# Optimization experiments

Measured on AMD Instinct MI355X. Metric: run time of the kernel, lower is better.

## Reference

```python
import jax, jax.numpy as jnp
import numpy as np

B, L, P, D = 512, 32, 256, 2


def hungarian(cost):
    """Min-cost assignment on an [n,n] numpy cost matrix (rows=pred, cols=target).
    Returns col[row]: target index assigned to each pred row (same as scipy
    linear_sum_assignment col_ind). Jonker-Volgenant style augmenting path."""
    n = cost.shape[0]
    INF = 1e18
    u = np.zeros(n + 1)
    v = np.zeros(n + 1)
    p = np.zeros(n + 1, dtype=np.int64)
    way = np.zeros(n + 1, dtype=np.int64)
    for i in range(1, n + 1):
        p[0] = i
        j0 = 0
        minv = np.full(n + 1, INF)
        used = np.zeros(n + 1, dtype=bool)
        while True:
            used[j0] = True
            i0 = p[j0]
            free = ~used[1:]
            cur = cost[i0 - 1, :] - u[i0] - v[1:]
            upd = free & (cur < minv[1:])
            m1 = minv[1:]
            m1[upd] = cur[upd]
            w1 = way[1:]
            w1[upd] = j0
            mfree = np.where(free, m1, INF)
            j1 = int(np.argmin(mfree)) + 1
            delta = mfree[j1 - 1]
            u[p[used]] += delta
            v[used] -= delta
            m1[free] -= delta
            j0 = j1
            if p[j0] == 0:
                break
        while j0:
            j1 = way[j0]
            p[j0] = p[j1]
            j0 = j1
    col = np.zeros(n, dtype=np.int64)
    for j in range(1, n + 1):
        col[p[j] - 1] = j - 1
    return col


def match_targets_np(pred_flat, tgt_flat, n_lines):
    """pred_flat/tgt_flat: np [B, L, P*D]; n_lines: np int [B].
    Replicates match_lines_sequence: Hungarian on pairwise squared L2 over the
    first n valid lines; unmatched rows stay zero (they are masked in the loss)."""
    out = np.zeros_like(pred_flat)
    for b in range(pred_flat.shape[0]):
        n = int(n_lines[b])
        if n == 1:
            out[b] = tgt_flat[b]
            continue
        pr = pred_flat[b, :n]
        tg = tgt_flat[b, :n]
        cost = ((pr[:, None, :] - tg[None, :, :]) ** 2).sum(-1)  # [pred, target]
        col = hungarian(cost)
        out[b, :n] = tgt_flat[b][col]
    return out


def setup_inputs() -> dict:
    key = jax.random.key(0)
    ks = jax.random.split(key, 5)
    point_pos_pred = jax.random.normal(ks[0], (B, L, P, D), jnp.float32)
    target_pos = jax.random.normal(ks[1], (B, L, P, D), jnp.float32)
    # probabilities in (0,1), bounded away from 0 so -log is finite
    line_prob_pred = jax.random.uniform(ks[2], (B, L, 2), jnp.float32) * 0.9 + 0.05
    n_lines = jax.random.randint(ks[3], (B,), 1, L + 1)
    line_masks = (jnp.arange(L)[None, :] < n_lines[:, None]).astype(jnp.float32)
    clf_line = jax.random.randint(ks[4], (B, L), 0, 2).astype(jnp.int32)
    point_masks = (line_masks[:, :, None] * jnp.ones((1, 1, P), jnp.float32))
    return {
        "point_pos_pred": point_pos_pred,
        "line_prob_pred": line_prob_pred,
        "target_pos": target_pos,
        "line_masks": line_masks,
        "clf_line": clf_line,
        "point_masks": point_masks,
    }


def reference(point_pos_pred, line_prob_pred, target_pos, line_masks, clf_line, point_masks):
    # --- Hungarian matching (host-side, non-differentiable, as in the original) ---
    pp = np.asarray(point_pos_pred).reshape(B, L, P * D)
    tp = np.asarray(target_pos).reshape(B, L, P * D)
    n_lines = np.asarray(line_masks).sum(axis=1).astype(np.int64)
    matched = jnp.asarray(match_targets_np(pp, tp, n_lines)).reshape(B, L, P, D)
    # --- masked MSE over (point, dim) ---
    sq = jnp.sum((point_pos_pred - matched) ** 2, axis=-1) * point_masks  # [B,L,P]
    mask_mse = jnp.sum(sq) / jnp.sum(point_masks)
    # --- masked NLL on line existence probabilities ---
    neg_log = -jnp.log(line_prob_pred).reshape(-1, 2)        # [B*L, 2]
    picked = jnp.take_along_axis(neg_log, clf_line.reshape(-1, 1), axis=1)
    clf_loss = jnp.sum(picked * line_masks.reshape(-1, 1)) / jnp.sum(line_masks)
    return (mask_mse, clf_loss)
```

## Files before the change

kernel.cpp:

```cpp
#include <hip/hip_runtime.h>
#include <cstdint>
#include <cstddef>

#define NB 512
#define NL 32
#define KD 512
#define KSLAB 128
#define PASS 128

__device__ __forceinline__ int swz128(int row, int ch) {
  int csw = (ch & ~15) | ((ch ^ (row >> 1)) & 15);
  return row * PASS + csw * 4;
}

__global__ __launch_bounds__(256, 2)
void cost_kernel(const float* __restrict__ pred, const float* __restrict__ tgt,
                 float* __restrict__ cost_part) {
  __shared__ float smem[8192];
  const int bid = blockIdx.x;
  const int b  = bid >> 2;
  const int ks = (bid & 3) * KSLAB;
  const int tid = threadIdx.x;
  float* predH = smem;
  float* tgtH  = smem + 4096;

  const int w = tid >> 6, l = tid & 63;
  const int ti = l >> 3, tj = l & 7;
  float acc[4][4];
#pragma unroll
  for (int a = 0; a < 4; ++a)
#pragma unroll
    for (int c2 = 0; c2 < 4; ++c2) acc[a][c2] = 0.f;

  const size_t base = (size_t)b * (NL * KD) + ks;
#pragma unroll
  for (int it = 0; it < 4; ++it) {
    int chunk = tid + it * 256;
    int row = chunk >> 5, ch = chunk & 31;
    const float4 pv = *reinterpret_cast<const float4*>(pred + base + (size_t)row * KD + ch * 4);
    const float4 tv = *reinterpret_cast<const float4*>(tgt  + base + (size_t)row * KD + ch * 4);
    int off = swz128(row, ch);
    *reinterpret_cast<float4*>(predH + off) = pv;
    *reinterpret_cast<float4*>(tgtH  + off) = tv;
  }
  __syncthreads();
#pragma unroll
  for (int c0 = 0; c0 < 8; ++c0) {
    const int c = (w << 3) + c0;
    float4 pr[4], tg[4];
#pragma unroll
    for (int r = 0; r < 4; ++r) {
      pr[r] = *reinterpret_cast<const float4*>(predH + swz128(4 * ti + r, c));
      tg[r] = *reinterpret_cast<const float4*>(tgtH  + swz128(4 * tj + r, c));
    }
#pragma unroll
    for (int a = 0; a < 4; ++a)
#pragma unroll
      for (int c2 = 0; c2 < 4; ++c2) {
        float d;
        d = pr[a].x - tg[c2].x; acc[a][c2] += d * d;
        d = pr[a].y - tg[c2].y; acc[a][c2] += d * d;
        d = pr[a].z - tg[c2].z; acc[a][c2] += d * d;
        d = pr[a].w - tg[c2].w; acc[a][c2] += d * d;
      }
  }
  __syncthreads();
#pragma unroll
  for (int a = 0; a < 4; ++a)
#pragma unroll
    for (int c2 = 0; c2 < 4; ++c2)
      smem[w * 1024 + (ti & 3) + 4 * tj + 32 * a + 128 * c2 + 512 * (ti >> 2)] = acc[a][c2];
  __syncthreads();
  const int ti2 = tid >> 5, a2 = (tid >> 3) & 3, tj2 = tid & 7;
  float ov[4];
#pragma unroll
  for (int k = 0; k < 4; ++k) {
    int ad = (ti2 & 3) + 4 * tj2 + 32 * a2 + 128 * k + 512 * (ti2 >> 2);
    ov[k] = (smem[ad] + smem[ad + 1024]) + (smem[ad + 2048] + smem[ad + 3072]);
  }
  *reinterpret_cast<float4*>(cost_part + (size_t)bid * 1024 + tid * 4) =
      make_float4(ov[0], ov[1], ov[2], ov[3]);
}

template<int CTRL, int RM>
__device__ __forceinline__ unsigned int dppumin(unsigned int x) {
  unsigned int m = (unsigned int)__builtin_amdgcn_update_dpp((int)x, (int)x, CTRL, RM, 0xf, false);
  return x < m ? x : m;
}
__device__ __forceinline__ unsigned int swz_xor16(unsigned int x) {
  return (unsigned int)__builtin_amdgcn_ds_swizzle((int)x, 0x401F);
}
__device__ __forceinline__ int bperm_i(int x, int srclane) {
  return __builtin_amdgcn_ds_bpermute(srclane << 2, x);
}
__device__ __forceinline__ float bperm_f(float x, int srclane) {
  return __int_as_float(__builtin_amdgcn_ds_bpermute(srclane << 2, __float_as_int(x)));
}
__device__ __forceinline__ float unsort_f(unsigned int y) {
  unsigned int x = (y & 0x80000000u) ? (y ^ 0x80000000u) : ~y;
  return __uint_as_float(x);
}

__global__ __launch_bounds__(64)
void hung_kernel(const float* __restrict__ cost_part,
                 const float* __restrict__ prob,
                 const float* __restrict__ lmask,
                 const int* __restrict__ clf,
                 float* __restrict__ part,
                 unsigned int* __restrict__ counter,
                 float* __restrict__ out) {
  __shared__ float cs[1024];
  const int b = blockIdx.x;
  const int lane = threadIdx.x;
  const int cl = lane & 31;

  {
    const float4* p0 = reinterpret_cast<const float4*>(cost_part + (size_t)(4 * b + 0) * 1024);
    const float4* p1 = reinterpret_cast<const float4*>(cost_part + (size_t)(4 * b + 1) * 1024);
    const float4* p2 = reinterpret_cast<const float4*>(cost_part + (size_t)(4 * b + 2) * 1024);
    const float4* p3 = reinterpret_cast<const float4*>(cost_part + (size_t)(4 * b + 3) * 1024);
    float4* cs4 = reinterpret_cast<float4*>(cs);
#pragma unroll
    for (int k = 0; k < 4; ++k) {
      int i = lane + 64 * k;
      float4 x0 = p0[i], x1 = p1[i], x2 = p2[i], x3 = p3[i];
      cs4[i] = make_float4((x0.x + x1.x) + (x2.x + x3.x),
                           (x0.y + x1.y) + (x2.y + x3.y),
                           (x0.z + x1.z) + (x2.z + x3.z),
                           (x0.w + x1.w) + (x2.w + x3.w));
    }
  }

  float lm = (lane < 32) ? lmask[b * 32 + lane] : 0.f;
  const int n = __popcll(__ballot(lm > 0.5f));
  float clfpart = 0.f;
  if (lane < 32 && lm > 0.5f) {
    int cc = clf[b * 32 + lane];
    clfpart = -logf(prob[(size_t)(b * 32 + lane) * 2 + cc]);
  }
  __syncthreads();

  const float FINF = 1e30f;
  const bool activecol = (cl < n);

  float u_r = 0.f, v_j = 0.f;
  int p_j = -1;

  for (int ri = 0; ri < n; ++ri) {
    int i0 = ri;
    bool usedc = false;
    bool usedr = (cl == ri);
    float rowv = cs[i0 * 32 + cl];
    float u0 = bperm_f(u_r, i0);
    while (true) {
      float key = rowv - v_j;
      float m = (activecol && !usedc) ? key : FINF;
      unsigned int mu = __float_as_uint(m);
      mu ^= (unsigned int)((int)mu >> 31) | 0x80000000u;
      unsigned int packed = (mu & 0xFFFFFFE0u) | (unsigned int)cl;
      packed = dppumin<0xB1, 0xf>(packed);
      packed = dppumin<0x4E, 0xf>(packed);
      packed = dppumin<0x124, 0xf>(packed);
      packed = dppumin<0x128, 0xf>(packed);
      { unsigned int o = swz_xor16(packed); packed = packed < o ? packed : o; }
      int j1 = (int)(packed & 31u);
      int pj1 = bperm_i(p_j, j1);
      int i0n = pj1 < 0 ? 0 : pj1;
      float rowv_n = cs[i0n * 32 + cl];
      float mnv = unsort_f(packed & 0xFFFFFFE0u);
      float delta = mnv - u0;
      if (usedr) u_r += delta;
      if (usedc) v_j -= delta;
      if (pj1 < 0) {
        if (cl == j1) p_j = ri;
        break;
      }
      usedc = usedc || (cl == j1);
      usedr = usedr || (cl == pj1);
      i0 = i0n;
      rowv = rowv_n;
      u0 = bperm_f(u_r, i0n);
    }
  }

  int pj = p_j < 0 ? 0 : p_j;
  float a = (lane < n) ? cs[pj * 32 + cl] : 0.f;
#pragma unroll
  for (int off = 32; off; off >>= 1) {
    a += __shfl_xor(a, off);
    clfpart += __shfl_xor(clfpart, off);
  }
  if (lane == 0) {
    part[b * 3 + 0] = a;
    part[b * 3 + 1] = clfpart;
    part[b * 3 + 2] = (float)n;
  }

  __threadfence();
  unsigned int t = 0;
  if (lane == 0) t = atomicAdd(counter, 1u);
  t = (unsigned int)__shfl((int)t, 0);
  if (t == NB - 1u) {
    __threadfence();
    volatile const float* vp = part;
    double csum = 0.0, lsum = 0.0, nsum = 0.0;
    for (int i = lane; i < NB; i += 64) {
      csum += (double)vp[i * 3 + 0];
      lsum += (double)vp[i * 3 + 1];
      nsum += (double)vp[i * 3 + 2];
    }
#pragma unroll
    for (int off = 32; off; off >>= 1) {
      csum += __shfl_xor(csum, off);
      lsum += __shfl_xor(lsum, off);
      nsum += __shfl_xor(nsum, off);
    }
    if (lane == 0) {
      out[0] = (float)(csum / (nsum * 256.0));
      out[1] = (float)(lsum / nsum);
    }
  }
}

extern "C" void kernel_launch(void* const* d_in, const int* in_sizes, int n_in,
                              void* d_out, int out_size, void* d_ws, size_t ws_size,
                              hipStream_t stream) {
  const float* pred = (const float*)d_in[0];
  const float* prob = (const float*)d_in[1];
  const float* tgt  = (const float*)d_in[2];
  const float* lm   = (const float*)d_in[3];
  const int*   clf  = (const int*)d_in[4];

  float* cost_part = (float*)d_ws;
  float* part = cost_part + (size_t)2048 * 1024;
  unsigned int* counter = (unsigned int*)(part + NB * 3);

  hipMemsetAsync(counter, 0, sizeof(unsigned int), stream);
  cost_kernel<<<NB * 4, 256, 0, stream>>>(pred, tgt, cost_part);
  hung_kernel<<<NB, 64, 0, stream>>>(cost_part, prob, lm, clf, part, counter,
                                     (float*)d_out);
}
```

Baseline: 70.14 us.

## Keep Hungarian column assignments in packed scalar registers and drop the counter memset

The per-column assignment array p_j moves out of a lane-distributed VGPR, which needed ds_bpermute lookups, into eight wave-uniform packed byte words. Lookups become scalar selects, and a free-column bitmask replaces the sentinel test. The wave min-reduction now ends in a DPP row broadcast plus readlane instead of ds_swizzle, and u0 is fetched with readlane. Resetting the counter moves into the cost kernel, which removes a separate memset launch. These changes shorten the latency of the serial augmenting-path loop at the cost of extra select logic.

```diff
diff --git a/kernel.cpp b/kernel.cpp
--- a/kernel.cpp
+++ b/kernel.cpp
@@ -15,9 +15,10 @@
 
 __global__ __launch_bounds__(256, 2)
 void cost_kernel(const float* __restrict__ pred, const float* __restrict__ tgt,
-                 float* __restrict__ cost_part) {
+                 float* __restrict__ cost_part, unsigned int* __restrict__ counter) {
   __shared__ float smem[8192];
   const int bid = blockIdx.x;
+  if (bid == 0 && threadIdx.x == 0) *counter = 0;
   const int b  = bid >> 2;
   const int ks = (bid & 3) * KSLAB;
   const int tid = threadIdx.x;
@@ -82,19 +83,22 @@
       make_float4(ov[0], ov[1], ov[2], ov[3]);
 }
 
+__device__ __forceinline__ float readlane_f(float x, int lane) {
+  return __int_as_float(__builtin_amdgcn_readlane(__float_as_int(x), lane));
+}
+
 template<int CTRL, int RM>
 __device__ __forceinline__ unsigned int dppumin(unsigned int x) {
   unsigned int m = (unsigned int)__builtin_amdgcn_update_dpp((int)x, (int)x, CTRL, RM, 0xf, false);
   return x < m ? x : m;
 }
-__device__ __forceinline__ unsigned int swz_xor16(unsigned int x) {
-  return (unsigned int)__builtin_amdgcn_ds_swizzle((int)x, 0x401F);
-}
-__device__ __forceinline__ int bperm_i(int x, int srclane) {
-  return __builtin_amdgcn_ds_bpermute(srclane << 2, x);
-}
-__device__ __forceinline__ float bperm_f(float x, int srclane) {
-  return __int_as_float(__builtin_amdgcn_ds_bpermute(srclane << 2, __float_as_int(x)));
+__device__ __forceinline__ unsigned int wave_umin32_bcast(unsigned int x) {
+  x = dppumin<0xB1, 0xf>(x);
+  x = dppumin<0x4E, 0xf>(x);
+  x = dppumin<0x124, 0xf>(x);
+  x = dppumin<0x128, 0xf>(x);
+  x = dppumin<0x142, 0xa>(x);
+  return (unsigned int)__builtin_amdgcn_readlane((int)x, 31);
 }
 __device__ __forceinline__ float unsort_f(unsigned int y) {
   unsigned int x = (y & 0x80000000u) ? (y ^ 0x80000000u) : ~y;
@@ -141,50 +145,74 @@
   __syncthreads();
 
   const float FINF = 1e30f;
-  const bool activecol = (cl < n);
+  const bool activecol = (lane < n);
 
   float u_r = 0.f, v_j = 0.f;
-  int p_j = -1;
+  unsigned int free32 = (n >= 32) ? 0xFFFFFFFFu : ((1u << n) - 1u);
+  unsigned int pp0 = 0, pp1 = 0, pp2 = 0, pp3 = 0, pp4 = 0, pp5 = 0, pp6 = 0, pp7 = 0;
 
   for (int ri = 0; ri < n; ++ri) {
     int i0 = ri;
     bool usedc = false;
-    bool usedr = (cl == ri);
+    bool usedr = (lane == ri);
     float rowv = cs[i0 * 32 + cl];
-    float u0 = bperm_f(u_r, i0);
+    float u0 = readlane_f(u_r, i0);
     while (true) {
       float key = rowv - v_j;
       float m = (activecol && !usedc) ? key : FINF;
       unsigned int mu = __float_as_uint(m);
       mu ^= (unsigned int)((int)mu >> 31) | 0x80000000u;
       unsigned int packed = (mu & 0xFFFFFFE0u) | (unsigned int)cl;
-      packed = dppumin<0xB1, 0xf>(packed);
-      packed = dppumin<0x4E, 0xf>(packed);
-      packed = dppumin<0x124, 0xf>(packed);
-      packed = dppumin<0x128, 0xf>(packed);
-      { unsigned int o = swz_xor16(packed); packed = packed < o ? packed : o; }
-      int j1 = (int)(packed & 31u);
-      int pj1 = bperm_i(p_j, j1);
-      int i0n = pj1 < 0 ? 0 : pj1;
+      unsigned int pmin = wave_umin32_bcast(packed);
+      int j1 = (int)(pmin & 31u);
+      unsigned int t0 = (j1 & 16) ? pp4 : pp0;
+      unsigned int t1 = (j1 & 16) ? pp5 : pp1;
+      unsigned int t2 = (j1 & 16) ? pp6 : pp2;
+      unsigned int t3 = (j1 & 16) ? pp7 : pp3;
+      unsigned int s0 = (j1 & 8) ? t2 : t0;
+      unsigned int s1 = (j1 & 8) ? t3 : t1;
+      unsigned int r0 = (j1 & 4) ? s1 : s0;
+      int pbyte = (int)((r0 >> ((j1 & 3) * 8)) & 0xFFu);
+      bool isfree = (free32 >> j1) & 1u;
+      int i0n = pbyte & 31;
       float rowv_n = cs[i0n * 32 + cl];
-      float mnv = unsort_f(packed & 0xFFFFFFE0u);
+      float mnv = unsort_f(pmin & 0xFFFFFFE0u);
       float delta = mnv - u0;
       if (usedr) u_r += delta;
       if (usedc) v_j -= delta;
-      if (pj1 < 0) {
-        if (cl == j1) p_j = ri;
+      if (isfree) {
+        unsigned int sh = (unsigned int)(j1 & 3) * 8u;
+        unsigned int msk = 0xFFu << sh;
+        unsigned int ins = ((unsigned int)ri) << sh;
+        int rsel = j1 >> 2;
+        pp0 = (rsel == 0) ? ((pp0 & ~msk) | ins) : pp0;
+        pp1 = (rsel == 1) ? ((pp1 & ~msk) | ins) : pp1;
+        pp2 = (rsel == 2) ? ((pp2 & ~msk) | ins) : pp2;
+        pp3 = (rsel == 3) ? ((pp3 & ~msk) | ins) : pp3;
+        pp4 = (rsel == 4) ? ((pp4 & ~msk) | ins) : pp4;
+        pp5 = (rsel == 5) ? ((pp5 & ~msk) | ins) : pp5;
+        pp6 = (rsel == 6) ? ((pp6 & ~msk) | ins) : pp6;
+        pp7 = (rsel == 7) ? ((pp7 & ~msk) | ins) : pp7;
+        free32 &= ~(1u << j1);
         break;
       }
-      usedc = usedc || (cl == j1);
-      usedr = usedr || (cl == pj1);
+      usedc = usedc || (lane == j1);
+      usedr = usedr || (lane == i0n);
       i0 = i0n;
       rowv = rowv_n;
-      u0 = bperm_f(u_r, i0n);
-    }
-  }
-
-  int pj = p_j < 0 ? 0 : p_j;
-  float a = (lane < n) ? cs[pj * 32 + cl] : 0.f;
+      u0 = readlane_f(u_r, i0);
+    }
+  }
+
+  unsigned int g0 = (lane & 16) ? pp4 : pp0;
+  unsigned int g1 = (lane & 16) ? pp5 : pp1;
+  unsigned int g2 = (lane & 16) ? pp6 : pp2;
+  unsigned int g3 = (lane & 16) ? pp7 : pp3;
+  unsigned int h0 = (lane & 8) ? g2 : g0;
+  unsigned int h1 = (lane & 8) ? g3 : g1;
+  unsigned int gr = (lane & 4) ? h1 : h0;
+  int pj = (int)((gr >> ((lane & 3) * 8)) & 0xFFu) & 31;
+  float a = activecol ? cs[pj * 32 + cl] : 0.f;
 #pragma unroll
   for (int off = 32; off; off >>= 1) {
     a += __shfl_xor(a, off);
@@ -235,8 +263,7 @@
   float* part = cost_part + (size_t)2048 * 1024;
   unsigned int* counter = (unsigned int*)(part + NB * 3);
 
-  hipMemsetAsync(counter, 0, sizeof(unsigned int), stream);
-  cost_kernel<<<NB * 4, 256, 0, stream>>>(pred, tgt, cost_part);
+  cost_kernel<<<NB * 4, 256, 0, stream>>>(pred, tgt, cost_part, counter);
   hung_kernel<<<NB, 64, 0, stream>>>(cost_part, prob, lm, clf, part, counter,
                                      (float*)d_out);
 }
```

Measured after the change: 65.34 us. 6.8% less time.
